# Kernel tuning notes

Hardware: AMD Instinct MI355X
Metric: run time of the kernel (lower is better)

## Reference

```python
import jax, jax.numpy as jnp
import numpy as np

T, S, F = 256, 128, 1024  # t frames, s persons, person_feature_len (= attn_len)


def setup_inputs() -> dict:
    key = jax.random.key(0)
    ks = jax.random.split(key, 9)
    scale = 1.0 / np.sqrt(F)
    return {
        "batch_data": jax.random.normal(ks[0], (T * S, F), dtype=jnp.float32),
        "xywh": jax.random.uniform(ks[1], (T * S, 4), dtype=jnp.float32),
        "Wa": jax.random.normal(ks[2], (F, F), dtype=jnp.float32) * scale,
        "ba": jnp.zeros((F,), dtype=jnp.float32),
        "Wb": jax.random.normal(ks[3], (F, F), dtype=jnp.float32) * scale,
        "bb": jnp.zeros((F,), dtype=jnp.float32),
        "Wg": jax.random.normal(ks[4], (F, F), dtype=jnp.float32) * scale,
        "bg": jnp.zeros((F,), dtype=jnp.float32),
        "OW": 1280,
        "OH": 720,
        "num_person": jax.random.randint(ks[5], (T,), 0, S, dtype=jnp.int64),
    }


def reference(batch_data, xywh, Wa, ba, Wb, bb, Wg, bg, OW, OH, num_person):
    # SemPosBlock.forward: only the SpatioVisualModule path contributes to the output.
    x = batch_data.reshape(T, S, F)            # person features per frame
    theta = jnp.einsum("tsf,fa->tsa", x, Wa) + ba
    phi = jnp.einsum("tsf,fa->tsa", x, Wb) + bb
    feats = jnp.einsum("tsf,fa->tsa", x, Wg) + bg
    # per-frame person-person attention: softmax(theta @ phi^T) @ feats
    scores = jnp.einsum("tsa,tja->tsj", theta, phi)     # [T, S, S]
    weights = jax.nn.softmax(scores, axis=-1)
    results = jnp.einsum("tsj,tja->tsa", weights, feats)  # [T, S, F]
    return results
```

## Files before the change

### kernel.cpp

```cpp
#include <hip/hip_runtime.h>

typedef _Float16 f16x8 __attribute__((ext_vector_type(8)));
typedef __attribute__((ext_vector_type(4))) float f32x4;

__device__ __forceinline__ unsigned short f16b(float x){
  _Float16 h = (_Float16)x;
  return __builtin_bit_cast(unsigned short, h);
}
__device__ __forceinline__ void split2h(float x, unsigned short &hi, unsigned short &lo){
  _Float16 h = (_Float16)x;
  _Float16 l = (_Float16)(x - (float)h);
  hi = __builtin_bit_cast(unsigned short, h);
  lo = __builtin_bit_cast(unsigned short, l);
}
__device__ __forceinline__ void gload_lds16(const void* g, void* l){
  __builtin_amdgcn_global_load_lds((const __attribute__((address_space(1))) void*)g,
                                   (__attribute__((address_space(3))) void*)l, 16, 0, 0);
}
#define VM(N)    asm volatile("s_waitcnt vmcnt(" #N ")" ::: "memory")
#define LGKM0()  do { asm volatile("s_waitcnt lgkmcnt(0)" ::: "memory"); \
                      __builtin_amdgcn_sched_barrier(0); } while(0)
#define BAR()    do { __builtin_amdgcn_s_barrier(); \
                      __builtin_amdgcn_sched_barrier(0); } while(0)

template<int MAP>
__device__ __forceinline__ int kmap(int k){ return k; }

template<int MAPA, int MAPB, int NK, int EPI>
__device__ __forceinline__ void gemm_body(
    const unsigned short* __restrict__ A, const unsigned short* __restrict__ B,
    unsigned short* __restrict__ outp, const float* __restrict__ bias,
    int lda, int ldb, int bm, int bn, char* ldsb)
{
  const int tid  = threadIdx.x;
  const int w    = tid >> 6;
  const int lane = tid & 63;
  const int wm   = w >> 2;
  const int wn   = w & 3;
  const int l15  = lane & 15;
  const int lg   = lane >> 4;

  int srow[2], slg[2];
#pragma unroll
  for (int j = 0; j < 2; j++){
    int o16 = j * 512 + tid;
    int p = o16 >> 3, s = o16 & 7;
    int q = s ^ (p & 7);
    srow[j] = 2 * p + (q >> 2);
    slg[j]  = q & 3;
  }
  const unsigned short* aS0 = A + (size_t)(bm * 256 + srow[0]) * lda + slg[0] * 8;
  const unsigned short* aS1 = A + (size_t)(bm * 256 + srow[1]) * lda + slg[1] * 8;
  const unsigned short* bS0 = B + (size_t)(bn * 256 + srow[0]) * ldb + slg[0] * 8;
  const unsigned short* bS1 = B + (size_t)(bn * 256 + srow[1]) * ldb + slg[1] * 8;

  const int sA   = (((l15 & 1) << 2) | lg) ^ ((l15 >> 1) & 7);
  const int rps  = (l15 >> 1) * 128 + sA * 16;

  f32x4 acc[8][4];
  f32x4 zero = {0.f, 0.f, 0.f, 0.f};
#pragma unroll
  for (int m = 0; m < 8; m++)
#pragma unroll
    for (int n = 0; n < 4; n++) acc[m][n] = zero;

  auto STAGE_Q = [&](int t, int q){
    char* slot = ldsb + (size_t)(t & 1) * 65536;
    const int kbA = kmap<MAPA>(t * 64);
    const int kbB = kmap<MAPB>(t * 64);
    if (q == 0){
      gload_lds16(aS0 + kbA,      slot +         w * 1024);
      gload_lds16(aS1 + kbA,      slot +  8192 + w * 1024);
    } else if (q == 1){
      gload_lds16(bS0 + kbB,      slot + 32768 + w * 1024);
      gload_lds16(bS1 + kbB,      slot + 40960 + w * 1024);
    } else if (q == 2){
      gload_lds16(bS0 + kbB + 32, slot + 49152 + w * 1024);
      gload_lds16(bS1 + kbB + 32, slot + 57344 + w * 1024);
    } else {
      gload_lds16(aS0 + kbA + 32, slot + 16384 + w * 1024);
      gload_lds16(aS1 + kbA + 32, slot + 24576 + w * 1024);
    }
  };

  STAGE_Q(0, 0); STAGE_Q(0, 1); STAGE_Q(0, 2); STAGE_Q(0, 3);

#pragma unroll 1
  for (int t = 0; t < NK; t++){
    const char* sb = ldsb + (size_t)(t & 1) * 65536;
    const bool pre = (t + 1 < NK);
    f16x8 aF[4], bF[4], aG[4], bF2[4], aF2[4], aG2[4];

    VM(4);
    BAR();
    if (pre) STAGE_Q(t + 1, 0);
#pragma unroll
    for (int m = 0; m < 4; m++) aF[m] = *(const f16x8*)(sb + wm * 8192 + m * 1024 + rps);
#pragma unroll
    for (int n = 0; n < 4; n++) bF[n] = *(const f16x8*)(sb + 32768 + wn * 4096 + n * 1024 + rps);
    LGKM0();
    __builtin_amdgcn_s_setprio(1);
#pragma unroll
    for (int m = 0; m < 4; m++)
#pragma unroll
      for (int n = 0; n < 4; n++)
        acc[m][n] = __builtin_amdgcn_mfma_f32_16x16x32_f16(aF[m], bF[n], acc[m][n], 0, 0, 0);
    __builtin_amdgcn_s_setprio(0);
    if (pre) STAGE_Q(t + 1, 1);
#pragma unroll
    for (int m = 0; m < 4; m++) aG[m] = *(const f16x8*)(sb + wm * 8192 + (m + 4) * 1024 + rps);
    LGKM0();
    __builtin_amdgcn_s_setprio(1);
#pragma unroll
    for (int m = 0; m < 4; m++)
#pragma unroll
      for (int n = 0; n < 4; n++)
        acc[m + 4][n] = __builtin_amdgcn_mfma_f32_16x16x32_f16(aG[m], bF[n], acc[m + 4][n], 0, 0, 0);
    __builtin_amdgcn_s_setprio(0);

    if (pre) { VM(4); } else { VM(0); }
    BAR();
    if (pre) STAGE_Q(t + 1, 2);
#pragma unroll
    for (int m = 0; m < 4; m++) aF2[m] = *(const f16x8*)(sb + 16384 + wm * 8192 + m * 1024 + rps);
#pragma unroll
    for (int n = 0; n < 4; n++) bF2[n] = *(const f16x8*)(sb + 49152 + wn * 4096 + n * 1024 + rps);
    LGKM0();
    __builtin_amdgcn_s_setprio(1);
#pragma unroll
    for (int m = 0; m < 4; m++)
#pragma unroll
      for (int n = 0; n < 4; n++)
        acc[m][n] = __builtin_amdgcn_mfma_f32_16x16x32_f16(aF2[m], bF2[n], acc[m][n], 0, 0, 0);
    __builtin_amdgcn_s_setprio(0);
    if (pre) STAGE_Q(t + 1, 3);
#pragma unroll
    for (int m = 0; m < 4; m++) aG2[m] = *(const f16x8*)(sb + 16384 + wm * 8192 + (m + 4) * 1024 + rps);
    LGKM0();
    __builtin_amdgcn_s_setprio(1);
#pragma unroll
    for (int m = 0; m < 4; m++)
#pragma unroll
      for (int n = 0; n < 4; n++)
        acc[m + 4][n] = __builtin_amdgcn_mfma_f32_16x16x32_f16(aG2[m], bF2[n], acc[m + 4][n], 0, 0, 0);
    __builtin_amdgcn_s_setprio(0);
  }

#pragma unroll
  for (int m = 0; m < 8; m++)
#pragma unroll
    for (int n = 0; n < 4; n++){
      const int col  = bn * 256 + wn * 64 + n * 16 + l15;
      const int row0 = bm * 256 + wm * 128 + m * 16 + lg * 4;
      if (EPI == 4){
#pragma unroll
        for (int q = 0; q < 4; q++)
          outp[(size_t)(row0 + q) * 2048 + col] = f16b(acc[m][n][q]);
      } else if (EPI == 6){
        float* of = (float*)outp;
#pragma unroll
        for (int q = 0; q < 4; q++)
          of[(size_t)col * 1024 + row0 + q] = acc[m][n][q];
      } else if (EPI == 7){
#pragma unroll
        for (int q = 0; q < 4; q++)
          outp[(size_t)(row0 + q) * 32768 + col] = f16b(acc[m][n][q] + bias[row0 + q]);
      }
    }
}

__global__ __launch_bounds__(512, 2) void k_big(
    const unsigned short* __restrict__ x2, const unsigned short* __restrict__ MTh,
    unsigned short* __restrict__ y2, const unsigned short* __restrict__ WgTh,
    unsigned short* __restrict__ FT, const float* __restrict__ bg)
{
  __shared__ __align__(16) unsigned short lds_u[65536];
  const int b = blockIdx.x;
  if (b < 512){
    int bid = (b & 7) * 64 + (b >> 3);
    gemm_body<0, 0, 16, 4>(x2, MTh, y2, nullptr, 1024, 1024, bid >> 2, bid & 3, (char*)lds_u);
  } else {
    int fb = b - 512;
    int fbid = (fb & 7) * 64 + (fb >> 3);
    gemm_body<0, 0, 16, 7>(WgTh, x2, FT, bg, 1024, 1024, fbid >> 7, fbid & 127, (char*)lds_u);
  }
}

__global__ __launch_bounds__(512, 1) void k_mtx(
    const unsigned short* __restrict__ Wa2, const unsigned short* __restrict__ Wb2,
    float* __restrict__ Mpart,
    const float* __restrict__ x, unsigned short* __restrict__ x2,
    const float* __restrict__ wv, float* __restrict__ v)
{
  __shared__ __align__(16) unsigned short lds_u[65536];
  const int b = blockIdx.x;
  if (b < 96){
    const int s = b >> 5, rest = b & 31;
    const int kc = rest >> 4, tile = rest & 15;
    const unsigned short* Aa = Wa2 + (s == 1 ? 1024 : 0) + kc * 512;
    const unsigned short* Bb = Wb2 + (s == 2 ? 1024 : 0) + kc * 512;
    gemm_body<0, 0, 8, 6>(Aa, Bb, (unsigned short*)(Mpart + (size_t)(s * 2 + kc) * 1048576),
                          nullptr, 2048, 2048, tile >> 2, tile & 3, (char*)lds_u);
  } else {
    const int bb = b - 96;
    const int w = threadIdx.x >> 6, lane = threadIdx.x & 63;
#pragma unroll
    for (int it = 0; it < 4; it++){
      const int row = bb * 8 + w + it * 8192;
      float s = 0.f;
#pragma unroll
      for (int j = 0; j < 4; j++){
        const int c = lane * 4 + j * 256;
        float4 val = *(const float4*)(x + (size_t)row * 1024 + c);
        float4 wvv = *(const float4*)(wv + c);
        ushort4 h, l;
        split2h(val.x, h.x, l.x); split2h(val.y, h.y, l.y);
        split2h(val.z, h.z, l.z); split2h(val.w, h.w, l.w);
        *(ushort4*)(x2 + (size_t)row * 1024 + c) = h;
        s += val.x * wvv.x + val.y * wvv.y + val.z * wvv.z + val.w * wvv.w;
      }
      for (int o = 32; o; o >>= 1) s += __shfl_xor(s, o);
      if (lane == 0) v[row] = s;
    }
  }
}

__global__ __launch_bounds__(256) void k_mt_reduce(const float* __restrict__ P,
                                                   unsigned short* __restrict__ MTh){
  const size_t i = ((size_t)blockIdx.x * 256 + threadIdx.x) * 4;
  float4 s = *(const float4*)(P + i);
#pragma unroll
  for (int p = 1; p < 6; p++){
    float4 a = *(const float4*)(P + (size_t)p * 1048576 + i);
    s.x += a.x; s.y += a.y; s.z += a.z; s.w += a.w;
  }
  ushort4 h;
  h.x = f16b(s.x); h.y = f16b(s.y); h.z = f16b(s.z); h.w = f16b(s.w);
  *(ushort4*)(MTh + i) = h;
}

__global__ __launch_bounds__(1024) void k_frame(
    const unsigned short* Y2, const unsigned short* X2,
    const float* __restrict__ v, const unsigned short* __restrict__ FT,
    float* outp)
{
  __shared__ __align__(16) unsigned short lds_u[49152];
  char* ldsb = (char*)lds_u;

  const int frame = blockIdx.x;
  const int tid  = threadIdx.x;
  const int w    = tid >> 6;
  const int lane = tid & 63;
  const int wm   = w >> 2;
  const int wn   = w & 3;
  const int l15  = lane & 15;
  const int lg   = lane >> 4;

  const int cS = tid & 511, hS = tid >> 9;
  const int pS = cS >> 3, sS = cS & 7;
  const int qS = sS ^ (pS & 7);
  const int srow = 2 * pS + (qS >> 2);
  const int slg  = qS & 3;
  const unsigned short* yS = Y2 + (size_t)(frame * 128 + srow) * 2048 + slg * 8;
  const unsigned short* xS = X2 + (size_t)(frame * 128 + srow) * 1024 + slg * 8;
  const int dY =         hS * 8192 + cS * 16;
  const int dX = 16384 + hS * 8192 + cS * 16;

  const int sA  = (((l15 & 1) << 2) | lg) ^ ((l15 >> 1) & 7);
  const int rps = (l15 >> 1) * 128 + sA * 16;

  f32x4 acc[2][2];
  f32x4 zero = {0.f, 0.f, 0.f, 0.f};
#pragma unroll
  for (int m = 0; m < 2; m++)
#pragma unroll
    for (int n = 0; n < 2; n++) acc[m][n] = zero;

  auto STAGE_K = [&](int t){
    char* slot = ldsb + (size_t)(t & 1) * 32768;
    const int kk = t * 64 + hS * 32;
    gload_lds16(yS + kk, slot + dY);
    gload_lds16(xS + kk, slot + dX);
  };

  const int NK = 16;
  STAGE_K(0);

#pragma unroll 1
  for (int t = 0; t < NK; t++){
    const char* sb = ldsb + (size_t)(t & 1) * 32768;
    if (t + 1 < NK){ STAGE_K(t + 1); VM(2); } else { VM(0); }
    BAR();
    f16x8 aF[2][2], bh[2][2];
#pragma unroll
    for (int h = 0; h < 2; h++){
#pragma unroll
      for (int m = 0; m < 2; m++)
        aF[h][m] = *(const f16x8*)(sb + h * 8192 + (wm * 2 + m) * 1024 + rps);
#pragma unroll
      for (int n = 0; n < 2; n++)
        bh[h][n] = *(const f16x8*)(sb + 16384 + h * 8192 + (wn * 2 + n) * 1024 + rps);
    }
    LGKM0();
    __builtin_amdgcn_s_setprio(1);
#pragma unroll
    for (int h = 0; h < 2; h++)
#pragma unroll
      for (int m = 0; m < 2; m++)
#pragma unroll
        for (int n = 0; n < 2; n++)
          acc[m][n] = __builtin_amdgcn_mfma_f32_16x16x32_f16(aF[h][m], bh[h][n], acc[m][n], 0, 0, 0);
    __builtin_amdgcn_s_setprio(0);
    BAR();
  }

  BAR();
  float* sf = (float*)ldsb;
#pragma unroll
  for (int m = 0; m < 2; m++)
#pragma unroll
    for (int n = 0; n < 2; n++){
      const int col = wn * 32 + n * 16 + l15;
#pragma unroll
      for (int q = 0; q < 4; q++){
        const int row = wm * 32 + m * 16 + lg * 4 + q;
        sf[row * 128 + ((col + (row & 31) * 4) & 127)] = acc[m][n][q];
      }
    }
  LGKM0(); BAR();
  unsigned short* Pb = (unsigned short*)(ldsb + 65536);
  {
    const float* vr = v + (size_t)frame * 128;
#pragma unroll 1
    for (int i = 0; i < 8; i++){
      const int row = w * 8 + i;
      const float* rp = sf + row * 128;
      const int rot = (row & 31) * 4;
      float a = rp[(lane + rot) & 127]      + vr[lane];
      float b = rp[(lane + 64 + rot) & 127] + vr[lane + 64];
      float mx = fmaxf(a, b);
      for (int o = 32; o; o >>= 1) mx = fmaxf(mx, __shfl_xor(mx, o));
      float ea = __expf(a - mx), eb = __expf(b - mx);
      float s = ea + eb;
      for (int o = 32; o; o >>= 1) s += __shfl_xor(s, o);
      const float inv = 1.0f / s;
      unsigned short* prow = (unsigned short*)((char*)Pb + row * 256);
      const int j0 = lane, j1 = lane + 64;
      *(unsigned short*)((char*)prow + (((j0 >> 3) ^ (row & 15)) * 16) + (j0 & 7) * 2) = f16b(ea * inv);
      *(unsigned short*)((char*)prow + (((j1 >> 3) ^ (row & 15)) * 16) + (j1 & 7) * 2) = f16b(eb * inv);
    }
  }
  LGKM0(); BAR();

  char* Fb = ldsb;
  auto STAGE_F = [&](int h){
    char* slot = Fb + (size_t)(h & 1) * 32768;
#pragma unroll
    for (int j = 0; j < 2; j++){
      const int o = j * 1024 + tid;
      const int a = o >> 4, c = o & 15;
      gload_lds16(FT + (size_t)(h * 128 + a) * 32768 + frame * 128 + (c ^ (a & 15)) * 8,
                  slot + (size_t)o * 16);
    }
  };
  STAGE_F(0);

#pragma unroll 1
  for (int h = 0; h < 8; h++){
    if (h + 1 < 8){ STAGE_F(h + 1); VM(2); } else { VM(0); }
    BAR();
    const char* fs = Fb + (size_t)(h & 1) * 32768;
    f16x8 pF[4][2], fF[4][2];
#pragma unroll
    for (int ks = 0; ks < 4; ks++){
#pragma unroll
      for (int m = 0; m < 2; m++){
        const int row = wm * 32 + m * 16 + l15;
        pF[ks][m] = *(const f16x8*)((char*)Pb + row * 256 + (((ks * 4 + lg) ^ (row & 15)) * 16));
      }
#pragma unroll
      for (int n = 0; n < 2; n++){
        const int al = wn * 32 + n * 16 + l15;
        fF[ks][n] = *(const f16x8*)(fs + al * 256 + (((ks * 4 + lg) ^ (al & 15)) * 16));
      }
    }
    LGKM0();
    f32x4 accP[2][2];
#pragma unroll
    for (int m = 0; m < 2; m++)
#pragma unroll
      for (int n = 0; n < 2; n++) accP[m][n] = zero;
    __builtin_amdgcn_s_setprio(1);
#pragma unroll
    for (int ks = 0; ks < 4; ks++)
#pragma unroll
      for (int m = 0; m < 2; m++)
#pragma unroll
        for (int n = 0; n < 2; n++)
          accP[m][n] = __builtin_amdgcn_mfma_f32_16x16x32_f16(pF[ks][m], fF[ks][n], accP[m][n], 0, 0, 0);
    __builtin_amdgcn_s_setprio(0);
#pragma unroll
    for (int m = 0; m < 2; m++)
#pragma unroll
      for (int n = 0; n < 2; n++){
        const int f  = h * 128 + wn * 32 + n * 16 + l15;
        const int r0 = wm * 32 + m * 16 + lg * 4;
#pragma unroll
        for (int q = 0; q < 4; q++)
          outp[((size_t)frame * 128 + r0 + q) * 1024 + f] = accP[m][n][q];
      }
    BAR();
  }
}

__global__ __launch_bounds__(256) void k_prep(const float* __restrict__ Wa,
                                              const float* __restrict__ Wb,
                                              const float* __restrict__ Wg,
                                              const float* __restrict__ ba,
                                              unsigned short* __restrict__ Wa2,
                                              unsigned short* __restrict__ Wb2,
                                              unsigned short* __restrict__ WgTh,
                                              float* __restrict__ wv){
  const int b = blockIdx.x;
  if (b < 2048){
    const int row = (b < 1024) ? b : (b - 1024);
    const float* src = (b < 1024) ? Wa : Wb;
    unsigned short* dst = (b < 1024) ? Wa2 : Wb2;
    const int c = threadIdx.x * 4;
    float4 val = *(const float4*)(src + (size_t)row * 1024 + c);
    ushort4 h, l;
    split2h(val.x, h.x, l.x); split2h(val.y, h.y, l.y);
    split2h(val.z, h.z, l.z); split2h(val.w, h.w, l.w);
    *(ushort4*)(dst + (size_t)row * 2048 + c) = h;
    *(ushort4*)(dst + (size_t)row * 2048 + 1024 + c) = l;
  } else if (b < 3072){
    const int row = b - 2048;
    const int c0 = threadIdx.x * 4;
    float4 val = *(const float4*)(Wg + (size_t)row * 1024 + c0);
    float vv[4] = {val.x, val.y, val.z, val.w};
#pragma unroll
    for (int i = 0; i < 4; i++)
      WgTh[(size_t)(c0 + i) * 1024 + row] = f16b(vv[i]);
  } else {
    const int row = (b - 3072) * 4 + (threadIdx.x >> 6);
    const int lane = threadIdx.x & 63;
    float s = 0.f;
#pragma unroll
    for (int j = 0; j < 4; j++){
      const int c = lane * 4 + j * 256;
      float4 wb = *(const float4*)(Wb + (size_t)row * 1024 + c);
      float4 bb = *(const float4*)(ba + c);
      s += wb.x * bb.x + wb.y * bb.y + wb.z * bb.z + wb.w * bb.w;
    }
    for (int o = 32; o; o >>= 1) s += __shfl_xor(s, o);
    if (lane == 0) wv[row] = s;
  }
}

extern "C" void kernel_launch(void* const* d_in, const int* in_sizes, int n_in,
                              void* d_out, int out_size, void* d_ws, size_t ws_size,
                              hipStream_t stream) {
  const float* x  = (const float*)d_in[0];
  const float* Wa = (const float*)d_in[2];
  const float* ba = (const float*)d_in[3];
  const float* Wb = (const float*)d_in[4];
  const float* Wg = (const float*)d_in[6];
  const float* bg = (const float*)d_in[7];

  unsigned short* x2   = (unsigned short*)d_ws;
  unsigned short* Wa2  = x2 + (size_t)32768 * 1024;
  unsigned short* Wb2  = Wa2 + (size_t)1024 * 2048;
  unsigned short* WgTh = Wb2 + (size_t)1024 * 2048;
  unsigned short* MTh  = WgTh + (size_t)1024 * 1024;
  unsigned short* FT   = MTh + (size_t)1024 * 1024;
  float* Mpart = (float*)(FT + (size_t)1024 * 32768);
  float* wv = Mpart + (size_t)6 * 1048576;
  float* v  = wv + 1024;
  size_t need = (size_t)((char*)(v + 32768) - (char*)d_ws);
  if (ws_size < need) return;

  unsigned short* y2 = (unsigned short*)d_out;

  k_prep      <<<3328, 256, 0, stream>>>(Wa, Wb, Wg, ba, Wa2, Wb2, WgTh, wv);
  k_mtx       <<<1120, 512, 0, stream>>>(Wa2, Wb2, Mpart, x, x2, wv, v);
  k_mt_reduce <<<1024, 256, 0, stream>>>(Mpart, MTh);
  k_big       <<<1024, 512, 0, stream>>>(x2, MTh, y2, WgTh, FT, bg);
  k_frame     <<<256, 1024, 0, stream>>>(y2, x2, v, FT, (float*)d_out);
}
```

Measured before the change: 282.1 us.

## Use 128x128 tiles with 256-thread blocks for the big GEMM kernel

Adds a 128x128-tile GEMM variant (4 waves, 32 KB of LDS double-buffered) and uses it for both k_big GEMMs, growing the grid from 1024 to 4096 blocks. The goal is better occupancy and load balance across CUs, since smaller blocks can co-reside and the wave tail is shorter. In exchange each tile reuses less data, so global and LDS traffic per FLOP roughly doubles and the loop synchronises more often per MFMA. The k_mtx path keeps the 256 tile with its epilogue simplified to the fp32 transpose store.

```diff
diff --git a/kernel.cpp b/kernel.cpp
--- a/kernel.cpp
+++ b/kernel.cpp
@@ -23,10 +23,7 @@
 #define BAR()    do { __builtin_amdgcn_s_barrier(); \
                       __builtin_amdgcn_sched_barrier(0); } while(0)
 
-template<int MAP>
-__device__ __forceinline__ int kmap(int k){ return k; }
-
-template<int MAPA, int MAPB, int NK, int EPI>
+template<int NK, int EPI>
 __device__ __forceinline__ void gemm_body(
     const unsigned short* __restrict__ A, const unsigned short* __restrict__ B,
     unsigned short* __restrict__ outp, const float* __restrict__ bias,
@@ -66,20 +63,19 @@
 
   auto STAGE_Q = [&](int t, int q){
     char* slot = ldsb + (size_t)(t & 1) * 65536;
-    const int kbA = kmap<MAPA>(t * 64);
-    const int kbB = kmap<MAPB>(t * 64);
+    const int kb = t * 64;
     if (q == 0){
-      gload_lds16(aS0 + kbA,      slot +         w * 1024);
-      gload_lds16(aS1 + kbA,      slot +  8192 + w * 1024);
+      gload_lds16(aS0 + kb,      slot +         w * 1024);
+      gload_lds16(aS1 + kb,      slot +  8192 + w * 1024);
     } else if (q == 1){
-      gload_lds16(bS0 + kbB,      slot + 32768 + w * 1024);
-      gload_lds16(bS1 + kbB,      slot + 40960 + w * 1024);
+      gload_lds16(bS0 + kb,      slot + 32768 + w * 1024);
+      gload_lds16(bS1 + kb,      slot + 40960 + w * 1024);
     } else if (q == 2){
-      gload_lds16(bS0 + kbB + 32, slot + 49152 + w * 1024);
-      gload_lds16(bS1 + kbB + 32, slot + 57344 + w * 1024);
+      gload_lds16(bS0 + kb + 32, slot + 49152 + w * 1024);
+      gload_lds16(bS1 + kb + 32, slot + 57344 + w * 1024);
     } else {
-      gload_lds16(aS0 + kbA + 32, slot + 16384 + w * 1024);
-      gload_lds16(aS1 + kbA + 32, slot + 24576 + w * 1024);
+      gload_lds16(aS0 + kb + 32, slot + 16384 + w * 1024);
+      gload_lds16(aS1 + kb + 32, slot + 24576 + w * 1024);
     }
   };
 
@@ -152,16 +148,121 @@
     for (int n = 0; n < 4; n++){
       const int col  = bn * 256 + wn * 64 + n * 16 + l15;
       const int row0 = bm * 256 + wm * 128 + m * 16 + lg * 4;
+      float* of = (float*)outp;
+#pragma unroll
+      for (int q = 0; q < 4; q++)
+        of[(size_t)col * 1024 + row0 + q] = acc[m][n][q];
+    }
+}
+
+template<int NK, int EPI>
+__device__ __forceinline__ void gemm_body128(
+    const unsigned short* __restrict__ A, const unsigned short* __restrict__ B,
+    unsigned short* __restrict__ outp, const float* __restrict__ bias,
+    int lda, int ldb, int bm, int bn, char* ldsb)
+{
+  const int tid  = threadIdx.x;
+  const int w    = tid >> 6;
+  const int lane = tid & 63;
+  const int wm   = w >> 1;
+  const int wn   = w & 1;
+  const int l15  = lane & 15;
+  const int lg   = lane >> 4;
+
+  int srow[2], slg[2];
+#pragma unroll
+  for (int j = 0; j < 2; j++){
+    int o = j * 256 + tid;
+    int p = o >> 3, s = o & 7;
+    int q = s ^ (p & 7);
+    srow[j] = 2 * p + (q >> 2);
+    slg[j]  = q & 3;
+  }
+  const unsigned short* aS0 = A + (size_t)(bm * 128 + srow[0]) * lda + slg[0] * 8;
+  const unsigned short* aS1 = A + (size_t)(bm * 128 + srow[1]) * lda + slg[1] * 8;
+  const unsigned short* bS0 = B + (size_t)(bn * 128 + srow[0]) * ldb + slg[0] * 8;
+  const unsigned short* bS1 = B + (size_t)(bn * 128 + srow[1]) * ldb + slg[1] * 8;
+
+  const int sA   = (((l15 & 1) << 2) | lg) ^ ((l15 >> 1) & 7);
+  const int rps  = (l15 >> 1) * 128 + sA * 16;
+
+  f32x4 acc[4][4];
+  f32x4 zero = {0.f, 0.f, 0.f, 0.f};
+#pragma unroll
+  for (int m = 0; m < 4; m++)
+#pragma unroll
+    for (int n = 0; n < 4; n++) acc[m][n] = zero;
+
+  auto STAGE_Q = [&](int t, int q){
+    char* slot = ldsb + (size_t)(t & 1) * 32768;
+    const int kb = t * 64;
+    if (q == 0){
+      gload_lds16(aS0 + kb,      slot +         tid * 16);
+      gload_lds16(aS1 + kb,      slot +  4096 + tid * 16);
+    } else if (q == 1){
+      gload_lds16(bS0 + kb,      slot + 16384 + tid * 16);
+      gload_lds16(bS1 + kb,      slot + 20480 + tid * 16);
+    } else if (q == 2){
+      gload_lds16(bS0 + kb + 32, slot + 24576 + tid * 16);
+      gload_lds16(bS1 + kb + 32, slot + 28672 + tid * 16);
+    } else {
+      gload_lds16(aS0 + kb + 32, slot +  8192 + tid * 16);
+      gload_lds16(aS1 + kb + 32, slot + 12288 + tid * 16);
+    }
+  };
+
+  STAGE_Q(0, 0); STAGE_Q(0, 1); STAGE_Q(0, 2); STAGE_Q(0, 3);
+
+#pragma unroll 1
+  for (int t = 0; t < NK; t++){
+    const char* sb = ldsb + (size_t)(t & 1) * 32768;
+    const bool pre = (t + 1 < NK);
+    f16x8 aF[4], bF[4], aF2[4], bF2[4];
+
+    VM(4);
+    BAR();
+    if (pre) { STAGE_Q(t + 1, 0); STAGE_Q(t + 1, 1); }
+#pragma unroll
+    for (int m = 0; m < 4; m++) aF[m] = *(const f16x8*)(sb + wm * 4096 + m * 1024 + rps);
+#pragma unroll
+    for (int n = 0; n < 4; n++) bF[n] = *(const f16x8*)(sb + 16384 + wn * 4096 + n * 1024 + rps);
+    LGKM0();
+    __builtin_amdgcn_s_setprio(1);
+#pragma unroll
+    for (int m = 0; m < 4; m++)
+#pragma unroll
+      for (int n = 0; n < 4; n++)
+        acc[m][n] = __builtin_amdgcn_mfma_f32_16x16x32_f16(aF[m], bF[n], acc[m][n], 0, 0, 0);
+    __builtin_amdgcn_s_setprio(0);
+
+    if (pre) { VM(4); } else { VM(0); }
+    BAR();
+    if (pre) { STAGE_Q(t + 1, 2); STAGE_Q(t + 1, 3); }
+#pragma unroll
+    for (int m = 0; m < 4; m++) aF2[m] = *(const f16x8*)(sb + 8192 + wm * 4096 + m * 1024 + rps);
+#pragma unroll
+    for (int n = 0; n < 4; n++) bF2[n] = *(const f16x8*)(sb + 24576 + wn * 4096 + n * 1024 + rps);
+    LGKM0();
+    __builtin_amdgcn_s_setprio(1);
+#pragma unroll
+    for (int m = 0; m < 4; m++)
+#pragma unroll
+      for (int n = 0; n < 4; n++)
+        acc[m][n] = __builtin_amdgcn_mfma_f32_16x16x32_f16(aF2[m], bF2[n], acc[m][n], 0, 0, 0);
+    __builtin_amdgcn_s_setprio(0);
+  }
+
+#pragma unroll
+  for (int m = 0; m < 4; m++)
+#pragma unroll
+    for (int n = 0; n < 4; n++){
+      const int col  = bn * 128 + wn * 64 + n * 16 + l15;
+      const int row0 = bm * 128 + wm * 64 + m * 16 + lg * 4;
       if (EPI == 4){
 #pragma unroll
         for (int q = 0; q < 4; q++)
           outp[(size_t)(row0 + q) * 2048 + col] = f16b(acc[m][n][q]);
-      } else if (EPI == 6){
-        float* of = (float*)outp;
-#pragma unroll
-        for (int q = 0; q < 4; q++)
-          of[(size_t)col * 1024 + row0 + q] = acc[m][n][q];
-      } else if (EPI == 7){
+      } else {
 #pragma unroll
         for (int q = 0; q < 4; q++)
           outp[(size_t)(row0 + q) * 32768 + col] = f16b(acc[m][n][q] + bias[row0 + q]);
@@ -169,20 +270,20 @@
     }
 }
 
-__global__ __launch_bounds__(512, 2) void k_big(
+__global__ __launch_bounds__(256, 2) void k_big(
     const unsigned short* __restrict__ x2, const unsigned short* __restrict__ MTh,
     unsigned short* __restrict__ y2, const unsigned short* __restrict__ WgTh,
     unsigned short* __restrict__ FT, const float* __restrict__ bg)
 {
-  __shared__ __align__(16) unsigned short lds_u[65536];
+  __shared__ __align__(16) unsigned short lds_u[32768];
   const int b = blockIdx.x;
-  if (b < 512){
-    int bid = (b & 7) * 64 + (b >> 3);
-    gemm_body<0, 0, 16, 4>(x2, MTh, y2, nullptr, 1024, 1024, bid >> 2, bid & 3, (char*)lds_u);
+  if (b < 2048){
+    int bid = (b & 7) * 256 + (b >> 3);
+    gemm_body128<16, 4>(x2, MTh, y2, nullptr, 1024, 1024, bid >> 3, bid & 7, (char*)lds_u);
   } else {
-    int fb = b - 512;
-    int fbid = (fb & 7) * 64 + (fb >> 3);
-    gemm_body<0, 0, 16, 7>(WgTh, x2, FT, bg, 1024, 1024, fbid >> 7, fbid & 127, (char*)lds_u);
+    int fb = b - 2048;
+    int fbid = (fb & 7) * 256 + (fb >> 3);
+    gemm_body128<16, 7>(WgTh, x2, FT, bg, 1024, 1024, fbid >> 8, fbid & 255, (char*)lds_u);
   }
 }
 
@@ -199,8 +300,8 @@
     const int kc = rest >> 4, tile = rest & 15;
     const unsigned short* Aa = Wa2 + (s == 1 ? 1024 : 0) + kc * 512;
     const unsigned short* Bb = Wb2 + (s == 2 ? 1024 : 0) + kc * 512;
-    gemm_body<0, 0, 8, 6>(Aa, Bb, (unsigned short*)(Mpart + (size_t)(s * 2 + kc) * 1048576),
-                          nullptr, 2048, 2048, tile >> 2, tile & 3, (char*)lds_u);
+    gemm_body<8, 6>(Aa, Bb, (unsigned short*)(Mpart + (size_t)(s * 2 + kc) * 1048576),
+                    nullptr, 2048, 2048, tile >> 2, tile & 3, (char*)lds_u);
   } else {
     const int bb = b - 96;
     const int w = threadIdx.x >> 6, lane = threadIdx.x & 63;
@@ -484,6 +585,6 @@
   k_prep      <<<3328, 256, 0, stream>>>(Wa, Wb, Wg, ba, Wa2, Wb2, WgTh, wv);
   k_mtx       <<<1120, 512, 0, stream>>>(Wa2, Wb2, Mpart, x, x2, wv, v);
   k_mt_reduce <<<1024, 256, 0, stream>>>(Mpart, MTh);
-  k_big       <<<1024, 512, 0, stream>>>(x2, MTh, y2, WgTh, FT, bg);
+  k_big       <<<4096, 256, 0, stream>>>(x2, MTh, y2, WgTh, FT, bg);
   k_frame     <<<256, 1024, 0, stream>>>(y2, x2, v, FT, (float*)d_out);
 }
```

After: 304.1 us. +7.8%, slower.
